# Optimization experiments

Hardware: AMD Instinct MI355X
Metric: run time of the kernel (lower is better)

## Reference

```python
import jax, jax.numpy as jnp
import numpy as np

N, D, T, ET, E = 100000, 128, 3, 4, 250000


def gru_cell(m, h, w_ih, w_hh, b_ih, b_hh):
    # torch.nn.GRUCell semantics
    gi = m @ w_ih.T + b_ih          # [N, 3D]
    gh = h @ w_hh.T + b_hh          # [N, 3D]
    i_r, i_z, i_n = jnp.split(gi, 3, axis=1)
    h_r, h_z, h_n = jnp.split(gh, 3, axis=1)
    r = jax.nn.sigmoid(i_r + h_r)
    z = jax.nn.sigmoid(i_z + h_z)
    n = jnp.tanh(i_n + r * h_n)
    return (1.0 - z) * n + z * h


def setup_inputs() -> dict:
    key = jax.random.key(0)
    ks = jax.random.split(key, 10)
    x = jax.random.normal(ks[0], (N, D), dtype=jnp.float32)
    edge_row = jax.random.randint(ks[1], (ET, E), 0, N, dtype=jnp.int32)
    edge_col = jax.random.randint(ks[2], (ET, E), 0, N, dtype=jnp.int32)
    edge_val = jnp.ones((ET, E), dtype=jnp.float32)
    xav = float(np.sqrt(6.0 / (D + D)))  # xavier_uniform per (D,D) slice
    weight = jax.random.uniform(ks[3], (T, ET, D, D), jnp.float32, -xav, xav)
    bias_w = jax.random.uniform(ks[4], (T, ET, D), jnp.float32, -0.01, 0.01)
    s = float(1.0 / np.sqrt(D))  # GRUCell default init range
    w_ih = jax.random.uniform(ks[5], (3 * D, D), jnp.float32, -s, s)
    w_hh = jax.random.uniform(ks[6], (3 * D, D), jnp.float32, -s, s)
    b_ih = jax.random.uniform(ks[7], (3 * D,), jnp.float32, -s, s)
    b_hh = jax.random.uniform(ks[8], (3 * D,), jnp.float32, -s, s)
    return {"x": x, "edge_row": edge_row, "edge_col": edge_col,
            "edge_val": edge_val, "weight": weight, "bias_w": bias_w,
            "w_ih": w_ih, "w_hh": w_hh, "b_ih": b_ih, "b_hh": b_hh}


def reference(x, edge_row, edge_col, edge_val, weight, bias_w, w_ih, w_hh, b_ih, b_hh):
    n_nodes = x.shape[0]
    h = x  # input_dim == out_channels, no zero-padding needed
    num_t = weight.shape[0]

    def agg_one(m_e, col_e, row_e, val_e):
        # sparse.mm: out[row] += val * m[col]
        msg = m_e[col_e] * val_e[:, None]                 # [E, D]
        return jax.ops.segment_sum(msg, row_e, num_segments=n_nodes)

    for t in range(num_t):
        # per-edge-type dense transform: [ET, N, D]
        m = jnp.einsum('nd,edf->enf', h, weight[t]) + bias_w[t][:, None, :]
        agg = jax.vmap(agg_one)(m, edge_col, edge_row, edge_val)  # [ET, N, D]
        m_sum = agg.sum(axis=0)                                    # [N, D]
        h = gru_cell(m_sum, h, w_ih, w_hh, b_ih, b_hh)
    return h
```

## Files before the change

kernel.cpp:

```cpp
#include <hip/hip_runtime.h>
#include <hip/hip_fp16.h>
#include <stdint.h>

#define NN  100000
#define DD  128
#define TT  3
#define ETT 4
#define EE  250000
#define NCH 49

typedef float  f32x4  __attribute__((ext_vector_type(4)));
typedef __bf16 bf16x8 __attribute__((ext_vector_type(8)));

__device__ __forceinline__ float bf2f(uint32_t u){ u <<= 16; return __builtin_bit_cast(float, u); }
__device__ __forceinline__ uint32_t f2bf(float f){
  uint32_t u = __builtin_bit_cast(uint32_t, f);
  return (u + 0x7FFFu + ((u >> 16) & 1u)) >> 16;
}
__device__ __forceinline__ float h2f(uint32_t u){ return __half2float(__ushort_as_half((uint16_t)u)); }
__device__ __forceinline__ uint32_t f2h(float f){ return (uint32_t)__half_as_ushort(__float2half(f)); }
__device__ __forceinline__ f32x4 mfma16(bf16x8 a, bf16x8 b, f32x4 c){
  return __builtin_amdgcn_mfma_f32_16x16x32_bf16(a, b, c, 0, 0, 0);
}

__global__ void k_count(const int* __restrict__ erow, const float* __restrict__ eval,
                        int* __restrict__ counts, float* __restrict__ degval){
  int idx = blockIdx.x * 256 + threadIdx.x;
  if (idx >= ETT * EE) return;
  int e = idx / EE;
  int row = erow[idx];
  atomicAdd(&counts[e * NN + row], 1);
  atomicAdd(&degval[e * NN + row], eval[idx]);
}

__global__ void k_blksum(const int* __restrict__ counts, int* __restrict__ bsum){
  const int b = blockIdx.x, e = b / NCH, c = b % NCH;
  const int* p = counts + e * NN + c * 2048;
  int lim = NN - c * 2048; if (lim > 2048) lim = 2048;
  const int t = threadIdx.x;
  int s = 0;
  #pragma unroll
  for (int i = 0; i < 8; ++i){
    int idx = i * 256 + t;
    if (idx < lim) s += p[idx];
  }
  #pragma unroll
  for (int d = 32; d; d >>= 1) s += __shfl_down(s, d);
  __shared__ int wsum[4];
  if ((t & 63) == 0) wsum[t >> 6] = s;
  __syncthreads();
  if (t == 0) bsum[b] = wsum[0] + wsum[1] + wsum[2] + wsum[3];
}

__global__ void k_scanp(const int* __restrict__ bsum, int* __restrict__ bexc,
                        int* __restrict__ offsets){
  const int t = threadIdx.x, wid = t >> 6, l = t & 63;
  int v = (l < NCH) ? bsum[wid * NCH + l] : 0;
  int x = v;
  #pragma unroll
  for (int d = 1; d < 64; d <<= 1){ int y = __shfl_up(x, d); if (l >= d) x += y; }
  if (l < NCH) bexc[wid * NCH + l] = x - v;
  if (l == NCH - 1) offsets[wid * (NN + 1) + NN] = x;
}

__global__ void k_apply(const int* __restrict__ counts, const int* __restrict__ bexc,
                        int* __restrict__ offsets){
  const int b = blockIdx.x, e = b / NCH, c = b % NCH;
  const int* p = counts + e * NN + c * 2048;
  int* off = offsets + e * (NN + 1) + c * 2048;
  int lim = NN - c * 2048; if (lim > 2048) lim = 2048;
  const int t = threadIdx.x, l = t & 63, wid = t >> 6;
  __shared__ int wt[4];
  int v[8], s = 0;
  #pragma unroll
  for (int i = 0; i < 8; ++i){
    int idx = t * 8 + i;
    v[i] = (idx < lim) ? p[idx] : 0; s += v[i];
  }
  int x = s;
  #pragma unroll
  for (int d = 1; d < 64; d <<= 1){ int y = __shfl_up(x, d); if (l >= d) x += y; }
  if (l == 63) wt[wid] = x;
  __syncthreads();
  int wexc = 0;
  #pragma unroll
  for (int k = 0; k < 4; ++k) if (k < wid) wexc += wt[k];
  int te = bexc[b] + wexc + (x - s);
  #pragma unroll
  for (int i = 0; i < 8; ++i){
    int idx = t * 8 + i;
    if (idx < lim) off[idx] = te;
    te += v[i];
  }
}

__global__ void k_fill(const int* __restrict__ erow, const int* __restrict__ ecol,
                       const float* __restrict__ eval, const int* __restrict__ offsets,
                       int* __restrict__ cursor, uint2* __restrict__ sedge){
  int idx = blockIdx.x * 256 + threadIdx.x;
  if (idx >= ETT * EE) return;
  int e = idx / EE;
  int row = erow[idx];
  int pos = atomicAdd(&cursor[e * NN + row], 1);
  int o = offsets[e * (NN + 1) + row] + pos;
  sedge[e * EE + o] = make_uint2((uint32_t)ecol[idx], __builtin_bit_cast(uint32_t, eval[idx]));
}

__global__ void k_conv_x(const float* __restrict__ x, uint16_t* __restrict__ hh){
  int idx = blockIdx.x * 256 + threadIdx.x;
  const float4* xp = (const float4*)x;
  float4 a = xp[idx * 2], b = xp[idx * 2 + 1];
  uint32_t p0 = f2h(a.x) | (f2h(a.y) << 16);
  uint32_t p1 = f2h(a.z) | (f2h(a.w) << 16);
  uint32_t p2 = f2h(b.x) | (f2h(b.y) << 16);
  uint32_t p3 = f2h(b.z) | (f2h(b.w) << 16);
  ((uint4*)hh)[idx] = make_uint4(p0, p1, p2, p3);
}

__global__ void k_conv_w(const float* __restrict__ weight, const float* __restrict__ wih,
                         const float* __restrict__ whh, const float* __restrict__ bih,
                         const float* __restrict__ bhh, uint16_t* __restrict__ wcatT,
                         uint16_t* __restrict__ wgru, float* __restrict__ bcomb){
  int idx = blockIdx.x * 256 + threadIdx.x;
  if (idx < TT * 128 * 512){
    int t = idx / 65536; int rem = idx - t * 65536;
    int f = rem >> 9; int u = rem & 511;
    int e = u >> 7; int d = u & 127;
    wcatT[idx] = (uint16_t)f2bf(weight[(((t * 4 + e) * 128 + d) << 7) + f]);
  }
  if (idx < 192 * 512){
    const int frag = idx >> 9, within = idx & 511;
    const int lane = within >> 3, i = within & 7;
    const int ks = frag & 3, bb = (frag >> 2) & 1, m = (frag >> 3) & 1;
    const int rem2 = frag >> 4;
    const int g = rem2 % 3, w = rem2 / 3;
    const int j = g * 128 + w * 32 + bb * 16 + (lane & 15);
    const int k = ks * 32 + (lane >> 4) * 8 + i;
    const float* src = m ? whh : wih;
    wgru[idx] = (uint16_t)f2bf(src[j * 128 + k]);
  }
  if (idx < 256) bcomb[idx] = bih[idx] + bhh[idx];
}

#define HACC8(val, u, base) \
  acc[base+0] += val * h2f(u.x & 0xffffu); acc[base+1] += val * h2f(u.x >> 16); \
  acc[base+2] += val * h2f(u.y & 0xffffu); acc[base+3] += val * h2f(u.y >> 16); \
  acc[base+4] += val * h2f(u.z & 0xffffu); acc[base+5] += val * h2f(u.z >> 16); \
  acc[base+6] += val * h2f(u.w & 0xffffu); acc[base+7] += val * h2f(u.w >> 16);

__global__ __launch_bounds__(256, 4) void k_step(
    const uint16_t* __restrict__ hsrc, uint16_t* __restrict__ hdst,
    float* __restrict__ out_f32, int last,
    const int* __restrict__ offsets, const uint2* __restrict__ sedge,
    const float* __restrict__ degval, const float* __restrict__ bias_w,
    const uint16_t* __restrict__ wcatT_t, int tstep,
    const uint16_t* __restrict__ wgru, const float* __restrict__ bcomb,
    const float* __restrict__ b_ih, const float* __restrict__ b_hh)
{
  __shared__ uint16_t aggT[32 * 512];
  __shared__ uint4 hT4[512];
  const int tid = threadIdx.x;
  const int node0 = blockIdx.x * 32;

  {
    const int nl = tid >> 3, q = tid & 7;
    const int n = node0 + nl;
    int se[4], ne[4];
    #pragma unroll
    for (int e = 0; e < ETT; ++e){
      se[e] = offsets[e * (NN + 1) + n];
      ne[e] = offsets[e * (NN + 1) + n + 1];
    }
    #pragma unroll 1
    for (int e = 0; e < ETT; ++e){
      float acc[16];
      #pragma unroll
      for (int i = 0; i < 16; ++i) acc[i] = 0.f;
      const int s = se[e], en = ne[e];
      const uint2* ep = sedge + (size_t)e * EE;
      #pragma unroll 1
      for (int i = s; i < en; i += 4){
        const int last_i = en - 1;
        const int i1 = (i + 1 < last_i) ? i + 1 : last_i;
        const int i2 = (i + 2 < last_i) ? i + 2 : last_i;
        const int i3 = (i + 3 < last_i) ? i + 3 : last_i;
        const uint2 cv0 = ep[i], cv1 = ep[i1], cv2 = ep[i2], cv3 = ep[i3];
        const float v0 = __builtin_bit_cast(float, cv0.y);
        const float v1 = (i + 1 <= last_i) ? __builtin_bit_cast(float, cv1.y) : 0.f;
        const float v2 = (i + 2 <= last_i) ? __builtin_bit_cast(float, cv2.y) : 0.f;
        const float v3 = (i + 3 <= last_i) ? __builtin_bit_cast(float, cv3.y) : 0.f;
        const uint4* p0 = (const uint4*)(hsrc + (size_t)cv0.x * DD + q * 16);
        const uint4* p1 = (const uint4*)(hsrc + (size_t)cv1.x * DD + q * 16);
        const uint4* p2 = (const uint4*)(hsrc + (size_t)cv2.x * DD + q * 16);
        const uint4* p3 = (const uint4*)(hsrc + (size_t)cv3.x * DD + q * 16);
        const uint4 a0 = p0[0], b0 = p0[1];
        const uint4 a1 = p1[0], b1 = p1[1];
        const uint4 a2 = p2[0], b2 = p2[1];
        const uint4 a3 = p3[0], b3 = p3[1];
        HACC8(v0, a0, 0); HACC8(v0, b0, 8);
        HACC8(v1, a1, 0); HACC8(v1, b1, 8);
        HACC8(v2, a2, 0); HACC8(v2, b2, 8);
        HACC8(v3, a3, 0); HACC8(v3, b3, 8);
      }
      #pragma unroll
      for (int c2 = 0; c2 < 2; ++c2){
        const int c  = e * 16 + q * 2 + c2;
        const int cs = c ^ (nl & 7);
        uint32_t p0 = f2bf(acc[c2*8+0]) | (f2bf(acc[c2*8+1]) << 16);
        uint32_t p1 = f2bf(acc[c2*8+2]) | (f2bf(acc[c2*8+3]) << 16);
        uint32_t p2 = f2bf(acc[c2*8+4]) | (f2bf(acc[c2*8+5]) << 16);
        uint32_t p3 = f2bf(acc[c2*8+6]) | (f2bf(acc[c2*8+7]) << 16);
        *(uint4*)&aggT[nl * 512 + cs * 8] = make_uint4(p0, p1, p2, p3);
      }
    }
  }
  __syncthreads();

  const int lane = tid & 63, w = tid >> 6;
  const int rlo = lane & 15, kg = lane >> 4;

  #pragma unroll
  for (int i = 0; i < 2; ++i){
    const int slot = tid * 2 + i;
    const int sn = slot >> 4, scs = slot & 15;
    const int sc = scs ^ (sn & 7);
    const uint4 hr = *(const uint4*)(hsrc + (size_t)(node0 + sn) * DD + sc * 8);
    uint32_t r0 = f2bf(h2f(hr.x & 0xffffu)) | (f2bf(h2f(hr.x >> 16)) << 16);
    uint32_t r1 = f2bf(h2f(hr.y & 0xffffu)) | (f2bf(h2f(hr.y >> 16)) << 16);
    uint32_t r2 = f2bf(h2f(hr.z & 0xffffu)) | (f2bf(h2f(hr.z >> 16)) << 16);
    uint32_t r3 = f2bf(h2f(hr.w & 0xffffu)) | (f2bf(h2f(hr.w >> 16)) << 16);
    hT4[slot] = make_uint4(r0, r1, r2, r3);
  }

  const int rt = w & 1, fh = w >> 1;
  const int rowA = rt * 16 + rlo;
  f32x4 C[4];
  #pragma unroll
  for (int i = 0; i < 4; ++i) C[i] = f32x4{0.f, 0.f, 0.f, 0.f};

  #pragma unroll
  for (int ks = 0; ks < 16; ++ks){
    const int cs = (ks * 4 + kg) ^ (rowA & 7);
    bf16x8 a = __builtin_bit_cast(bf16x8, *(const uint4*)&aggT[rowA * 512 + cs * 8]);
    #pragma unroll
    for (int ft = 0; ft < 4; ++ft){
      const int f = fh * 64 + ft * 16 + rlo;
      bf16x8 b = __builtin_bit_cast(bf16x8, *(const uint4*)(wcatT_t + (size_t)f * 512 + ks * 32 + kg * 8));
      C[ft] = mfma16(a, b, C[ft]);
    }
  }

  const float* bwt = bias_w + tstep * (ETT * DD);
  float dv[4][4];
  #pragma unroll
  for (int r = 0; r < 4; ++r){
    const int n2 = node0 + rt * 16 + kg * 4 + r;
    #pragma unroll
    for (int e = 0; e < 4; ++e) dv[e][r] = degval[e * NN + n2];
  }
  __syncthreads();

  uint16_t* mT = aggT;
  #pragma unroll
  for (int ft = 0; ft < 4; ++ft){
    const int f = fh * 64 + ft * 16 + rlo;
    const float b0 = bwt[f], b1 = bwt[128 + f], b2 = bwt[256 + f], b3 = bwt[384 + f];
    #pragma unroll
    for (int r = 0; r < 4; ++r){
      const int n2l = rt * 16 + kg * 4 + r;
      const float bias = dv[0][r]*b0 + dv[1][r]*b1 + dv[2][r]*b2 + dv[3][r]*b3;
      mT[n2l * 128 + (((f >> 3) ^ (n2l & 7)) << 3) + (f & 7)] = (uint16_t)f2bf(C[ft][r] + bias);
    }
  }
  __syncthreads();

  const uint4* mT4 = (const uint4*)aggT;
  #pragma unroll
  for (int bb = 0; bb < 2; ++bb){
    f32x4 acc[3][2][2];
    #pragma unroll
    for (int g = 0; g < 3; ++g)
      #pragma unroll
      for (int m = 0; m < 2; ++m)
        #pragma unroll
        for (int ns = 0; ns < 2; ++ns) acc[g][m][ns] = f32x4{0.f,0.f,0.f,0.f};

    #pragma unroll
    for (int ks = 0; ks < 4; ++ks){
      bf16x8 fa[3], fb[3];
      #pragma unroll
      for (int g = 0; g < 3; ++g){
        const int fragA = (((w * 3 + g) * 2 + 0) * 2 + bb) * 4 + ks;
        const int fragB = (((w * 3 + g) * 2 + 1) * 2 + bb) * 4 + ks;
        fa[g] = __builtin_bit_cast(bf16x8, *(const uint4*)(wgru + fragA * 512 + lane * 8));
        fb[g] = __builtin_bit_cast(bf16x8, *(const uint4*)(wgru + fragB * 512 + lane * 8));
      }
      #pragma unroll
      for (int ns = 0; ns < 2; ++ns){
        const int node = ns * 16 + rlo;
        const int cs = (ks * 4 + kg) ^ (node & 7);
        const bf16x8 bm = __builtin_bit_cast(bf16x8, mT4[node * 16 + cs]);
        const bf16x8 bh = __builtin_bit_cast(bf16x8, hT4[node * 16 + cs]);
        #pragma unroll
        for (int g = 0; g < 3; ++g){
          acc[g][0][ns] = mfma16(fa[g], bm, acc[g][0][ns]);
          acc[g][1][ns] = mfma16(fb[g], bh, acc[g][1][ns]);
        }
      }
    }

    const int d0 = w * 32 + bb * 16 + kg * 4;
    const f32x4 brz = *(const f32x4*)(bcomb + d0);
    const f32x4 bzz = *(const f32x4*)(bcomb + 128 + d0);
    const f32x4 bin = *(const f32x4*)(b_ih + 256 + d0);
    const f32x4 bhn = *(const f32x4*)(b_hh + 256 + d0);
    #pragma unroll
    for (int ns = 0; ns < 2; ++ns){
      const int node = node0 + ns * 16 + rlo;
      const uint2 hov = *(const uint2*)(hsrc + (size_t)node * DD + d0);
      const float ho[4] = { h2f(hov.x & 0xffffu), h2f(hov.x >> 16),
                            h2f(hov.y & 0xffffu), h2f(hov.y >> 16) };
      float hv[4];
      #pragma unroll
      for (int r = 0; r < 4; ++r){
        const float rg = 1.f / (1.f + __expf(-(acc[0][0][ns][r] + acc[0][1][ns][r] + brz[r])));
        const float zg = 1.f / (1.f + __expf(-(acc[1][0][ns][r] + acc[1][1][ns][r] + bzz[r])));
        const float xa = (acc[2][0][ns][r] + bin[r]) + rg * (acc[2][1][ns][r] + bhn[r]);
        const float ng = 1.f - 2.f / (__expf(2.f * xa) + 1.f);
        hv[r] = (1.f - zg) * ng + zg * ho[r];
      }
      if (last){
        *(f32x4*)(out_f32 + (size_t)node * DD + d0) = f32x4{hv[0], hv[1], hv[2], hv[3]};
      } else {
        uint32_t q0 = f2h(hv[0]) | (f2h(hv[1]) << 16);
        uint32_t q1 = f2h(hv[2]) | (f2h(hv[3]) << 16);
        *(uint2*)(hdst + (size_t)node * DD + d0) = make_uint2(q0, q1);
      }
    }
  }
}

extern "C" void kernel_launch(void* const* d_in, const int* in_sizes, int n_in,
                              void* d_out, int out_size, void* d_ws, size_t ws_size,
                              hipStream_t stream) {
  const float* x      = (const float*)d_in[0];
  const int*   erow   = (const int*)d_in[1];
  const int*   ecol   = (const int*)d_in[2];
  const float* eval   = (const float*)d_in[3];
  const float* weight = (const float*)d_in[4];
  const float* bias_w = (const float*)d_in[5];
  const float* wih    = (const float*)d_in[6];
  const float* whh    = (const float*)d_in[7];
  const float* bih    = (const float*)d_in[8];
  const float* bhh    = (const float*)d_in[9];
  float* out = (float*)d_out;
  char* ws = (char*)d_ws;

  size_t o = 0;
  auto alloc = [&](size_t bytes)->char*{ char* p = ws + o; o += (bytes + 255) & ~(size_t)255; return p; };
  int*      counts  = (int*)     alloc((size_t)ETT * NN * 4);
  int*      cursor  = (int*)     alloc((size_t)ETT * NN * 4);
  float*    degval  = (float*)   alloc((size_t)ETT * NN * 4);
  int*      offsets = (int*)     alloc((size_t)ETT * (NN + 1) * 4);
  int*      bsum    = (int*)     alloc((size_t)ETT * NCH * 4);
  int*      bexc    = (int*)     alloc((size_t)ETT * NCH * 4);
  uint2*    sedge   = (uint2*)   alloc((size_t)ETT * EE * 8);
  uint16_t* hh0     = (uint16_t*)alloc((size_t)NN * DD * 2);
  uint16_t* hh1     = (uint16_t*)alloc((size_t)NN * DD * 2);
  uint16_t* wcatT   = (uint16_t*)alloc((size_t)TT * 128 * 512 * 2);
  uint16_t* wgru    = (uint16_t*)alloc((size_t)192 * 512 * 2);
  float*    bcomb   = (float*)   alloc((size_t)256 * 4);
  (void)ws_size; (void)in_sizes; (void)n_in; (void)out_size;

  hipMemsetAsync(counts, 0, (size_t)3 * ETT * NN * 4, stream);

  k_count<<<(ETT * EE + 255) / 256, 256, 0, stream>>>(erow, eval, counts, degval);
  k_blksum<<<ETT * NCH, 256, 0, stream>>>(counts, bsum);
  k_scanp<<<1, 256, 0, stream>>>(bsum, bexc, offsets);
  k_apply<<<ETT * NCH, 256, 0, stream>>>(counts, bexc, offsets);
  k_fill<<<(ETT * EE + 255) / 256, 256, 0, stream>>>(erow, ecol, eval, offsets, cursor, sedge);
  k_conv_x<<<(NN * DD / 8) / 256, 256, 0, stream>>>(x, hh0);
  k_conv_w<<<(TT * 128 * 512 + 255) / 256, 256, 0, stream>>>(weight, wih, whh, bih, bhh,
                                                             wcatT, wgru, bcomb);

  uint16_t* hs = hh0;
  uint16_t* hd = hh1;
  for (int t = 0; t < TT; ++t){
    const int last = (t == TT - 1);
    k_step<<<NN / 32, 256, 0, stream>>>(hs, hd, out, last, offsets, sedge, degval,
                                        bias_w, wcatT + (size_t)t * 65536, t,
                                        wgru, bcomb, bih, bhh);
    uint16_t* tmp = hs; hs = hd; hd = tmp;
  }
}
```

Measured before the change: 688.8 us.

## Use fma_mix for half gather-accumulate, reuse LDS for h tile, raise occupancy

New measurement: 767.6 us. 1.11x slower.

```diff
diff --git a/kernel.cpp b/kernel.cpp
--- a/kernel.cpp
+++ b/kernel.cpp
@@ -21,6 +21,14 @@
 __device__ __forceinline__ uint32_t f2h(float f){ return (uint32_t)__half_as_ushort(__float2half(f)); }
 __device__ __forceinline__ f32x4 mfma16(bf16x8 a, bf16x8 b, f32x4 c){
   return __builtin_amdgcn_mfma_f32_16x16x32_bf16(a, b, c, 0, 0, 0);
+}
+__device__ __forceinline__ void fmamix_lo(float& acc, uint32_t h, float v){
+  asm("v_fma_mix_f32 %0, %1, %2, %0 op_sel:[0,0,0] op_sel_hi:[1,0,0]"
+      : "+v"(acc) : "v"(h), "v"(v));
+}
+__device__ __forceinline__ void fmamix_hi(float& acc, uint32_t h, float v){
+  asm("v_fma_mix_f32 %0, %1, %2, %0 op_sel:[1,0,0] op_sel_hi:[1,0,0]"
+      : "+v"(acc) : "v"(h), "v"(v));
 }
 
 __global__ void k_count(const int* __restrict__ erow, const float* __restrict__ eval,
@@ -143,12 +151,12 @@
 }
 
 #define HACC8(val, u, base) \
-  acc[base+0] += val * h2f(u.x & 0xffffu); acc[base+1] += val * h2f(u.x >> 16); \
-  acc[base+2] += val * h2f(u.y & 0xffffu); acc[base+3] += val * h2f(u.y >> 16); \
-  acc[base+4] += val * h2f(u.z & 0xffffu); acc[base+5] += val * h2f(u.z >> 16); \
-  acc[base+6] += val * h2f(u.w & 0xffffu); acc[base+7] += val * h2f(u.w >> 16);
-
-__global__ __launch_bounds__(256, 4) void k_step(
+  fmamix_lo(acc[base+0], u.x, val); fmamix_hi(acc[base+1], u.x, val); \
+  fmamix_lo(acc[base+2], u.y, val); fmamix_hi(acc[base+3], u.y, val); \
+  fmamix_lo(acc[base+4], u.z, val); fmamix_hi(acc[base+5], u.z, val); \
+  fmamix_lo(acc[base+6], u.w, val); fmamix_hi(acc[base+7], u.w, val);
+
+__global__ __launch_bounds__(256, 5) void k_step(
     const uint16_t* __restrict__ hsrc, uint16_t* __restrict__ hdst,
     float* __restrict__ out_f32, int last,
     const int* __restrict__ offsets, const uint2* __restrict__ sedge,
@@ -158,37 +166,31 @@
     const float* __restrict__ b_ih, const float* __restrict__ b_hh)
 {
   __shared__ uint16_t aggT[32 * 512];
-  __shared__ uint4 hT4[512];
   const int tid = threadIdx.x;
   const int node0 = blockIdx.x * 32;
 
   {
     const int nl = tid >> 3, q = tid & 7;
     const int n = node0 + nl;
-    int se[4], ne[4];
-    #pragma unroll
-    for (int e = 0; e < ETT; ++e){
-      se[e] = offsets[e * (NN + 1) + n];
-      ne[e] = offsets[e * (NN + 1) + n + 1];
-    }
-    #pragma unroll 1
+    #pragma unroll
     for (int e = 0; e < ETT; ++e){
       float acc[16];
       #pragma unroll
       for (int i = 0; i < 16; ++i) acc[i] = 0.f;
-      const int s = se[e], en = ne[e];
+      const int s  = offsets[e * (NN + 1) + n];
+      const int en = offsets[e * (NN + 1) + n + 1];
       const uint2* ep = sedge + (size_t)e * EE;
       #pragma unroll 1
       for (int i = s; i < en; i += 4){
-        const int last_i = en - 1;
-        const int i1 = (i + 1 < last_i) ? i + 1 : last_i;
-        const int i2 = (i + 2 < last_i) ? i + 2 : last_i;
-        const int i3 = (i + 3 < last_i) ? i + 3 : last_i;
+        const int lastI = en - 1;
+        const int i1 = (i + 1 < lastI) ? i + 1 : lastI;
+        const int i2 = (i + 2 < lastI) ? i + 2 : lastI;
+        const int i3 = (i + 3 < lastI) ? i + 3 : lastI;
         const uint2 cv0 = ep[i], cv1 = ep[i1], cv2 = ep[i2], cv3 = ep[i3];
         const float v0 = __builtin_bit_cast(float, cv0.y);
-        const float v1 = (i + 1 <= last_i) ? __builtin_bit_cast(float, cv1.y) : 0.f;
-        const float v2 = (i + 2 <= last_i) ? __builtin_bit_cast(float, cv2.y) : 0.f;
-        const float v3 = (i + 3 <= last_i) ? __builtin_bit_cast(float, cv3.y) : 0.f;
+        const float v1 = (i + 1 <= lastI) ? __builtin_bit_cast(float, cv1.y) : 0.f;
+        const float v2 = (i + 2 <= lastI) ? __builtin_bit_cast(float, cv2.y) : 0.f;
+        const float v3 = (i + 3 <= lastI) ? __builtin_bit_cast(float, cv3.y) : 0.f;
         const uint4* p0 = (const uint4*)(hsrc + (size_t)cv0.x * DD + q * 16);
         const uint4* p1 = (const uint4*)(hsrc + (size_t)cv1.x * DD + q * 16);
         const uint4* p2 = (const uint4*)(hsrc + (size_t)cv2.x * DD + q * 16);
@@ -219,17 +221,13 @@
   const int lane = tid & 63, w = tid >> 6;
   const int rlo = lane & 15, kg = lane >> 4;
 
-  #pragma unroll
-  for (int i = 0; i < 2; ++i){
-    const int slot = tid * 2 + i;
-    const int sn = slot >> 4, scs = slot & 15;
-    const int sc = scs ^ (sn & 7);
-    const uint4 hr = *(const uint4*)(hsrc + (size_t)(node0 + sn) * DD + sc * 8);
-    uint32_t r0 = f2bf(h2f(hr.x & 0xffffu)) | (f2bf(h2f(hr.x >> 16)) << 16);
-    uint32_t r1 = f2bf(h2f(hr.y & 0xffffu)) | (f2bf(h2f(hr.y >> 16)) << 16);
-    uint32_t r2 = f2bf(h2f(hr.z & 0xffffu)) | (f2bf(h2f(hr.z >> 16)) << 16);
-    uint32_t r3 = f2bf(h2f(hr.w & 0xffffu)) | (f2bf(h2f(hr.w >> 16)) << 16);
-    hT4[slot] = make_uint4(r0, r1, r2, r3);
+  uint4 hr0, hr1;
+  {
+    const int slot0 = tid * 2, slot1 = tid * 2 + 1;
+    const int sn0 = slot0 >> 4, scs0 = slot0 & 15, sc0 = scs0 ^ (sn0 & 7);
+    const int sn1 = slot1 >> 4, scs1 = slot1 & 15, sc1 = scs1 ^ (sn1 & 7);
+    hr0 = *(const uint4*)(hsrc + (size_t)(node0 + sn0) * DD + sc0 * 8);
+    hr1 = *(const uint4*)(hsrc + (size_t)(node0 + sn1) * DD + sc1 * 8);
   }
 
   const int rt = w & 1, fh = w >> 1;
@@ -272,9 +270,22 @@
       mT[n2l * 128 + (((f >> 3) ^ (n2l & 7)) << 3) + (f & 7)] = (uint16_t)f2bf(C[ft][r] + bias);
     }
   }
+  {
+    uint32_t r0 = f2bf(h2f(hr0.x & 0xffffu)) | (f2bf(h2f(hr0.x >> 16)) << 16);
+    uint32_t r1 = f2bf(h2f(hr0.y & 0xffffu)) | (f2bf(h2f(hr0.y >> 16)) << 16);
+    uint32_t r2 = f2bf(h2f(hr0.z & 0xffffu)) | (f2bf(h2f(hr0.z >> 16)) << 16);
+    uint32_t r3 = f2bf(h2f(hr0.w & 0xffffu)) | (f2bf(h2f(hr0.w >> 16)) << 16);
+    ((uint4*)aggT)[512 + tid * 2] = make_uint4(r0, r1, r2, r3);
+    r0 = f2bf(h2f(hr1.x & 0xffffu)) | (f2bf(h2f(hr1.x >> 16)) << 16);
+    r1 = f2bf(h2f(hr1.y & 0xffffu)) | (f2bf(h2f(hr1.y >> 16)) << 16);
+    r2 = f2bf(h2f(hr1.z & 0xffffu)) | (f2bf(h2f(hr1.z >> 16)) << 16);
+    r3 = f2bf(h2f(hr1.w & 0xffffu)) | (f2bf(h2f(hr1.w >> 16)) << 16);
+    ((uint4*)aggT)[512 + tid * 2 + 1] = make_uint4(r0, r1, r2, r3);
+  }
   __syncthreads();
 
   const uint4* mT4 = (const uint4*)aggT;
+  const uint4* hT4 = ((const uint4*)aggT) + 512;
   #pragma unroll
   for (int bb = 0; bb < 2; ++bb){
     f32x4 acc[3][2][2];
```
